# Kernel tuning notes

Measured on AMD Instinct MI355X. Metric: run time of the kernel, lower is better.

## Reference

```python
import jax, jax.numpy as jnp
import numpy as np

N_NODES = 100000
N_EDGES = 640000
HIDDEN = 128
OUT = 128


def _graph_conv(x, edge_index, W_rel, b_rel, W_root):
    # PyG GraphConv (aggr='add'):
    #   out[i] = x[i] @ W_root.T + (sum_{(j->i) in E} x[j]) @ W_rel.T + b_rel
    src, dst = edge_index[0], edge_index[1]
    agg = jax.ops.segment_sum(x[src], dst, num_segments=N_NODES)  # [N, d_in]
    return x @ W_root.T + agg @ W_rel.T + b_rel


def setup_inputs() -> dict:
    key = jax.random.key(0)
    ks = jax.random.split(key, 10)
    x = jax.random.normal(ks[0], (N_NODES, HIDDEN), dtype=jnp.float32)
    edge_index = jax.random.randint(ks[1], (2, N_EDGES), 0, N_NODES, dtype=jnp.int64)
    s = 1.0 / np.sqrt(HIDDEN)
    def w(k, o, i):
        return jax.random.normal(k, (o, i), dtype=jnp.float32) * s
    return {
        "x": x,
        "edge_index": edge_index,
        "W_rel0": w(ks[2], HIDDEN, HIDDEN), "b0": jnp.zeros((HIDDEN,), jnp.float32), "W_root0": w(ks[3], HIDDEN, HIDDEN),
        "W_rel1": w(ks[4], HIDDEN, HIDDEN), "b1": jnp.zeros((HIDDEN,), jnp.float32), "W_root1": w(ks[5], HIDDEN, HIDDEN),
        "W_rel2": w(ks[6], OUT, HIDDEN),    "b2": jnp.zeros((OUT,), jnp.float32),    "W_root2": w(ks[7], OUT, HIDDEN),
    }


def reference(x, edge_index, W_rel0, b0, W_root0, W_rel1, b1, W_root1, W_rel2, b2, W_root2):
    h = jax.nn.relu(_graph_conv(x, edge_index, W_rel0, b0, W_root0))
    h = jax.nn.relu(_graph_conv(h, edge_index, W_rel1, b1, W_root1))
    h = _graph_conv(h, edge_index, W_rel2, b2, W_root2)  # no ReLU on end_conv
    return h
```

## Files before the change

### kernel.cpp

```cpp
#include <hip/hip_runtime.h>

constexpr int HID = 128;

typedef __attribute__((ext_vector_type(8))) short bf16x8;
typedef __attribute__((ext_vector_type(4))) float f32x4;

__device__ __forceinline__ unsigned short f2bf(float f) {
    unsigned int u = __float_as_uint(f);
    u += 0x7fffu + ((u >> 16) & 1u);
    return (unsigned short)(u >> 16);
}
__device__ __forceinline__ float bf_lo(unsigned int v) { return __uint_as_float(v << 16); }
__device__ __forceinline__ float bf_hi(unsigned int v) { return __uint_as_float(v & 0xffff0000u); }

__device__ __forceinline__ void gload16(const void* g, void* l) {
    __builtin_amdgcn_global_load_lds(
        (const __attribute__((address_space(1))) void*)g,
        (__attribute__((address_space(3))) void*)l, 16, 0, 0);
}

__global__ __launch_bounds__(256) void cvt_x_k(
    const float* __restrict__ in, unsigned short* __restrict__ out, int n4)
{
    const int i = blockIdx.x * 256 + threadIdx.x;
    if (i >= n4) return;
    const float4 v = reinterpret_cast<const float4*>(in)[i];
    ushort4 o;
    o.x = f2bf(v.x); o.y = f2bf(v.y); o.z = f2bf(v.z); o.w = f2bf(v.w);
    reinterpret_cast<ushort4*>(out)[i] = o;
}

struct WPtrs { const float* s[6]; unsigned short* d[6]; };
__global__ __launch_bounds__(256) void cvt_w_k(WPtrs p)
{
    const int which = blockIdx.y;
    const int i = blockIdx.x * 256 + threadIdx.x;
    if (i >= (HID * HID) / 4) return;
    const float4 v = reinterpret_cast<const float4*>(p.s[which])[i];
    ushort4 o;
    o.x = f2bf(v.x); o.y = f2bf(v.y); o.z = f2bf(v.z); o.w = f2bf(v.w);
    reinterpret_cast<ushort4*>(p.d[which])[i] = o;
}

__global__ __launch_bounds__(256) void hist_rank_k(
    const int* __restrict__ dst, int* __restrict__ deg,
    int* __restrict__ rank, int nEdges)
{
    const int i = blockIdx.x * blockDim.x + threadIdx.x;
    if (i < nEdges) rank[i] = atomicAdd(&deg[dst[i]], 1);
}

__global__ __launch_bounds__(256) void scan1_k(
    const int* __restrict__ deg, int* __restrict__ part,
    int* __restrict__ blockSums, int n)
{
    __shared__ int s[256];
    const int t = threadIdx.x;
    const int i = blockIdx.x * 1024 + t * 4;
    const int e0 = (i + 0 < n) ? deg[i + 0] : 0;
    const int e1 = (i + 1 < n) ? deg[i + 1] : 0;
    const int e2 = (i + 2 < n) ? deg[i + 2] : 0;
    const int e3 = (i + 3 < n) ? deg[i + 3] : 0;
    const int local = e0 + e1 + e2 + e3;
    s[t] = local;
    __syncthreads();
    for (int off = 1; off < 256; off <<= 1) {
        int v = 0;
        if (t >= off) v = s[t - off];
        __syncthreads();
        if (t >= off) s[t] += v;
        __syncthreads();
    }
    const int incl = s[t];
    int excl = incl - local;
    if (t == 255) blockSums[blockIdx.x] = incl;
    if (i + 0 < n) part[i + 0] = excl; excl += e0;
    if (i + 1 < n) part[i + 1] = excl; excl += e1;
    if (i + 2 < n) part[i + 2] = excl; excl += e2;
    if (i + 3 < n) part[i + 3] = excl;
}

__global__ __launch_bounds__(128) void scan2_k(int* __restrict__ blockSums, int nb)
{
    __shared__ int s[128];
    const int t = threadIdx.x;
    const int v = (t < nb) ? blockSums[t] : 0;
    s[t] = v;
    __syncthreads();
    for (int off = 1; off < 128; off <<= 1) {
        int u = 0;
        if (t >= off) u = s[t - off];
        __syncthreads();
        if (t >= off) s[t] += u;
        __syncthreads();
    }
    if (t < nb) blockSums[t] = s[t] - v;
}

__global__ __launch_bounds__(256) void scan3_k(
    const int* __restrict__ part, const int* __restrict__ blockSums,
    int* __restrict__ rowStart, int n, int nEdges)
{
    const int i = blockIdx.x * blockDim.x + threadIdx.x;
    if (i < n) rowStart[i] = part[i] + blockSums[i >> 10];
    if (i == n) rowStart[n] = nEdges;
}

__global__ __launch_bounds__(256) void fill2_k(
    const int* __restrict__ src, const int* __restrict__ dst,
    const int* __restrict__ rank, const int* __restrict__ rowStart,
    int* __restrict__ eSrc, int nEdges)
{
    const int i = blockIdx.x * blockDim.x + threadIdx.x;
    if (i < nEdges) eSrc[rowStart[dst[i]] + rank[i]] = src[i];
}

__global__ __launch_bounds__(256) void gather_agg_k(
    const unsigned short* __restrict__ feat,
    const int*            __restrict__ rowStart,
    const int*            __restrict__ eSrc,
    unsigned short*       __restrict__ agg,
    int nNodes)
{
    const int wid  = (blockIdx.x * blockDim.x + threadIdx.x) >> 6;
    const int lane = threadIdx.x & 63;
    const int g    = lane >> 4;
    const int sl   = lane & 15;
    const int node = wid * 4 + g;
    if (node >= nNodes) return;

    const int beg = rowStart[node];
    const int end = rowStart[node + 1];
    const size_t colOff = (size_t)sl * 8;
    const int gbase = g << 4;

    float acc[8];
#pragma unroll
    for (int q = 0; q < 8; ++q) acc[q] = 0.f;

    for (int base = beg; base < end; base += 16) {
        const int cnt = min(16, end - base);
        const int si = eSrc[base + min(sl, cnt - 1)];

        int j = 0;
        for (; j + 8 <= cnt; j += 8) {
            uint4 v[8];
#pragma unroll
            for (int q = 0; q < 8; ++q) {
                const int s = __shfl(si, gbase + j + q, 64);
                v[q] = *reinterpret_cast<const uint4*>(feat + (size_t)s * HID + colOff);
            }
#pragma unroll
            for (int q = 0; q < 8; ++q) {
                acc[0] += bf_lo(v[q].x); acc[1] += bf_hi(v[q].x);
                acc[2] += bf_lo(v[q].y); acc[3] += bf_hi(v[q].y);
                acc[4] += bf_lo(v[q].z); acc[5] += bf_hi(v[q].z);
                acc[6] += bf_lo(v[q].w); acc[7] += bf_hi(v[q].w);
            }
        }
        if (j + 4 <= cnt) {
            uint4 v[4];
#pragma unroll
            for (int q = 0; q < 4; ++q) {
                const int s = __shfl(si, gbase + j + q, 64);
                v[q] = *reinterpret_cast<const uint4*>(feat + (size_t)s * HID + colOff);
            }
#pragma unroll
            for (int q = 0; q < 4; ++q) {
                acc[0] += bf_lo(v[q].x); acc[1] += bf_hi(v[q].x);
                acc[2] += bf_lo(v[q].y); acc[3] += bf_hi(v[q].y);
                acc[4] += bf_lo(v[q].z); acc[5] += bf_hi(v[q].z);
                acc[6] += bf_lo(v[q].w); acc[7] += bf_hi(v[q].w);
            }
            j += 4;
        }
        if (j + 2 <= cnt) {
            uint4 v[2];
#pragma unroll
            for (int q = 0; q < 2; ++q) {
                const int s = __shfl(si, gbase + j + q, 64);
                v[q] = *reinterpret_cast<const uint4*>(feat + (size_t)s * HID + colOff);
            }
#pragma unroll
            for (int q = 0; q < 2; ++q) {
                acc[0] += bf_lo(v[q].x); acc[1] += bf_hi(v[q].x);
                acc[2] += bf_lo(v[q].y); acc[3] += bf_hi(v[q].y);
                acc[4] += bf_lo(v[q].z); acc[5] += bf_hi(v[q].z);
                acc[6] += bf_lo(v[q].w); acc[7] += bf_hi(v[q].w);
            }
            j += 2;
        }
        if (j < cnt) {
            const int s = __shfl(si, gbase + j, 64);
            const uint4 v = *reinterpret_cast<const uint4*>(feat + (size_t)s * HID + colOff);
            acc[0] += bf_lo(v.x); acc[1] += bf_hi(v.x);
            acc[2] += bf_lo(v.y); acc[3] += bf_hi(v.y);
            acc[4] += bf_lo(v.z); acc[5] += bf_hi(v.z);
            acc[6] += bf_lo(v.w); acc[7] += bf_hi(v.w);
        }
    }

    uint4 o;
    o.x = (unsigned int)f2bf(acc[0]) | ((unsigned int)f2bf(acc[1]) << 16);
    o.y = (unsigned int)f2bf(acc[2]) | ((unsigned int)f2bf(acc[3]) << 16);
    o.z = (unsigned int)f2bf(acc[4]) | ((unsigned int)f2bf(acc[5]) << 16);
    o.w = (unsigned int)f2bf(acc[6]) | ((unsigned int)f2bf(acc[7]) << 16);
    *reinterpret_cast<uint4*>(agg + (size_t)node * HID + colOff) = o;
}

__device__ __forceinline__ void stage_tile(
    const unsigned short* __restrict__ F, const unsigned short* __restrict__ Wm,
    unsigned short* XsBuf, unsigned short* WsBuf,
    int w, int stHalf, int rsub, int srcColB, int k0, int row0, int rowMax)
{
    if (w < 2) {
#pragma unroll
        for (int q = 0; q < 8; ++q) {
            const int row = stHalf * 64 + q * 8 + rsub;
            const int gr  = min(row0 + row, rowMax);
            gload16((const char*)(F + (size_t)gr * HID + k0) + srcColB,
                    XsBuf + (stHalf * 64 + q * 8) * 64);
        }
    } else {
#pragma unroll
        for (int q = 0; q < 8; ++q) {
            const int row = stHalf * 64 + q * 8 + rsub;
            gload16((const char*)(Wm + (size_t)row * HID + k0) + srcColB,
                    WsBuf + (stHalf * 64 + q * 8) * 64);
        }
    }
}

template <int MODE>
__global__ __launch_bounds__(256) void gemm_mfma_k(
    const unsigned short* __restrict__ X,
    const unsigned short* __restrict__ AGG,
    const unsigned short* __restrict__ Wroot,
    const unsigned short* __restrict__ Wrel,
    const float*          __restrict__ bias,
    void*                 __restrict__ OUTv,
    int nRows)
{
    __shared__ unsigned short Xs[2][128 * 64];
    __shared__ unsigned short Ws[2][128 * 64];

    const int tid  = threadIdx.x;
    const int lane = tid & 63;
    const int w    = tid >> 6;
    const int row0 = blockIdx.x * 128;

    const int wr = w >> 1, wc = w & 1;
    const int R0 = wr * 64, C0 = wc * 64;
    const int lr = lane & 15, lk = lane >> 4;
    const int swz = (lr & 7) << 4;

    const int rsub    = lane >> 3;
    const int srcColB = (((lane & 7) ^ rsub) << 4);
    const int stHalf  = w & 1;
    const int rowMax  = nRows - 1;

    f32x4 acc[4][4];
#pragma unroll
    for (int m = 0; m < 4; ++m)
#pragma unroll
        for (int n = 0; n < 4; ++n) acc[m][n] = f32x4{0.f, 0.f, 0.f, 0.f};

    stage_tile(X, Wroot, Xs[0], Ws[0], w, stHalf, rsub, srcColB, 0, row0, rowMax);

#pragma unroll
    for (int t = 0; t < 4; ++t) {
        const int cur = t & 1;
        if (t < 3) {
            const unsigned short* Fn = (t + 1 < 2) ? X : AGG;
            const unsigned short* Wn = (t + 1 < 2) ? Wroot : Wrel;
            stage_tile(Fn, Wn, Xs[cur ^ 1], Ws[cur ^ 1],
                       w, stHalf, rsub, srcColB, ((t + 1) & 1) * 64, row0, rowMax);
            asm volatile("s_waitcnt vmcnt(8)" ::: "memory");
        } else {
            asm volatile("s_waitcnt vmcnt(0)" ::: "memory");
        }
        __builtin_amdgcn_s_barrier();

#pragma unroll
        for (int ks = 0; ks < 2; ++ks) {
            bf16x8 af[4], bfr[4];
            const int kB = (ks * 64 + lk * 16) ^ swz;
#pragma unroll
            for (int m = 0; m < 4; ++m) {
                const int row = R0 + m * 16 + lr;
                af[m] = *reinterpret_cast<const bf16x8*>((const char*)Xs[cur] + row * 128 + kB);
            }
#pragma unroll
            for (int n = 0; n < 4; ++n) {
                const int col = C0 + n * 16 + lr;
                bfr[n] = *reinterpret_cast<const bf16x8*>((const char*)Ws[cur] + col * 128 + kB);
            }
#pragma unroll
            for (int m = 0; m < 4; ++m)
#pragma unroll
                for (int n = 0; n < 4; ++n)
                    acc[m][n] = __builtin_amdgcn_mfma_f32_16x16x32_bf16(
                        af[m], bfr[n], acc[m][n], 0, 0, 0);
        }
        if (t < 3) __builtin_amdgcn_s_barrier();
    }

    float bv[4];
#pragma unroll
    for (int n = 0; n < 4; ++n) bv[n] = bias[C0 + n * 16 + lr];

#pragma unroll
    for (int m = 0; m < 4; ++m) {
        const int rbase = row0 + R0 + m * 16 + lk * 4;
#pragma unroll
        for (int j = 0; j < 4; ++j) {
            const int r = rbase + j;
            if (r < nRows) {
#pragma unroll
                for (int n = 0; n < 4; ++n) {
                    const int col = C0 + n * 16 + lr;
                    float v = acc[m][n][j] + bv[n];
                    if (MODE == 0) {
                        v = fmaxf(v, 0.f);
                        ((unsigned short*)OUTv)[(size_t)r * HID + col] = f2bf(v);
                    } else {
                        ((float*)OUTv)[(size_t)r * HID + col] = v;
                    }
                }
            }
        }
    }
}

extern "C" void kernel_launch(void* const* d_in, const int* in_sizes, int n_in,
                              void* d_out, int out_size, void* d_ws, size_t ws_size,
                              hipStream_t stream)
{
    const float* x      = (const float*)d_in[0];
    const int*   ei     = (const int*)  d_in[1];
    const float* Wrel0  = (const float*)d_in[2];
    const float* b0     = (const float*)d_in[3];
    const float* Wroot0 = (const float*)d_in[4];
    const float* Wrel1  = (const float*)d_in[5];
    const float* b1     = (const float*)d_in[6];
    const float* Wroot1 = (const float*)d_in[7];
    const float* Wrel2  = (const float*)d_in[8];
    const float* b2     = (const float*)d_in[9];
    const float* Wroot2 = (const float*)d_in[10];

    const int nNodes = in_sizes[0] / HID;
    const int nEdges = in_sizes[1] / 2;
    const int* srcI = ei;
    const int* dstI = ei + nEdges;
    const size_t nF = (size_t)nNodes * HID;

    float* OUT = (float*)d_out;

    unsigned short* xb   = (unsigned short*)d_ws;
    unsigned short* hA   = xb + nF;
    unsigned short* hB   = hA + nF;
    unsigned short* aggb = hB + nF;
    unsigned short* wb   = aggb + nF;
    int* deg       = (int*)(wb + 6 * HID * HID);
    int* part      = deg + nNodes;
    int* rowStart  = part + nNodes;
    int* blockSums = rowStart + nNodes + 1;
    int* rank      = blockSums + 128;
    int* eSrc      = rank + nEdges;

    unsigned short* Wrel0b  = wb + 0 * HID * HID;
    unsigned short* Wroot0b = wb + 1 * HID * HID;
    unsigned short* Wrel1b  = wb + 2 * HID * HID;
    unsigned short* Wroot1b = wb + 3 * HID * HID;
    unsigned short* Wrel2b  = wb + 4 * HID * HID;
    unsigned short* Wroot2b = wb + 5 * HID * HID;

    cvt_x_k<<<(int)((nF / 4 + 255) / 256), 256, 0, stream>>>(x, xb, (int)(nF / 4));
    WPtrs wp;
    wp.s[0] = Wrel0;  wp.d[0] = Wrel0b;
    wp.s[1] = Wroot0; wp.d[1] = Wroot0b;
    wp.s[2] = Wrel1;  wp.d[2] = Wrel1b;
    wp.s[3] = Wroot1; wp.d[3] = Wroot1b;
    wp.s[4] = Wrel2;  wp.d[4] = Wrel2b;
    wp.s[5] = Wroot2; wp.d[5] = Wroot2b;
    cvt_w_k<<<dim3(16, 6), 256, 0, stream>>>(wp);

    const int nb = (nNodes + 1023) / 1024;
    hipMemsetAsync(deg, 0, (size_t)nNodes * sizeof(int), stream);
    hist_rank_k<<<(nEdges + 255) / 256, 256, 0, stream>>>(dstI, deg, rank, nEdges);
    scan1_k<<<nb, 256, 0, stream>>>(deg, part, blockSums, nNodes);
    scan2_k<<<1, 128, 0, stream>>>(blockSums, nb);
    scan3_k<<<(nNodes + 256) / 256, 256, 0, stream>>>(part, blockSums, rowStart, nNodes, nEdges);
    fill2_k<<<(nEdges + 255) / 256, 256, 0, stream>>>(srcI, dstI, rank, rowStart, eSrc, nEdges);

    const int aGrid = (int)(((size_t)(nNodes + 3) / 4 * 64 + 255) / 256);
    const int gGrid = (nNodes + 127) / 128;

    gather_agg_k<<<aGrid, 256, 0, stream>>>(xb, rowStart, eSrc, aggb, nNodes);
    gemm_mfma_k<0><<<gGrid, 256, 0, stream>>>(xb, aggb, Wroot0b, Wrel0b, b0, hA, nNodes);

    gather_agg_k<<<aGrid, 256, 0, stream>>>(hA, rowStart, eSrc, aggb, nNodes);
    gemm_mfma_k<0><<<gGrid, 256, 0, stream>>>(hA, aggb, Wroot1b, Wrel1b, b1, hB, nNodes);

    gather_agg_k<<<aGrid, 256, 0, stream>>>(hB, rowStart, eSrc, aggb, nNodes);
    gemm_mfma_k<1><<<gGrid, 256, 0, stream>>>(hB, aggb, Wroot2b, Wrel2b, b2, OUT, nNodes);
}
```

Before: 206.8 us.

## Fuse neighbor gather into MFMA GEMM and merge prep kernels

```diff
diff --git a/kernel.cpp b/kernel.cpp
--- a/kernel.cpp
+++ b/kernel.cpp
@@ -19,35 +19,36 @@
         (__attribute__((address_space(3))) void*)l, 16, 0, 0);
 }
 
-__global__ __launch_bounds__(256) void cvt_x_k(
-    const float* __restrict__ in, unsigned short* __restrict__ out, int n4)
-{
-    const int i = blockIdx.x * 256 + threadIdx.x;
-    if (i >= n4) return;
-    const float4 v = reinterpret_cast<const float4*>(in)[i];
-    ushort4 o;
-    o.x = f2bf(v.x); o.y = f2bf(v.y); o.z = f2bf(v.z); o.w = f2bf(v.w);
-    reinterpret_cast<ushort4*>(out)[i] = o;
-}
-
-struct WPtrs { const float* s[6]; unsigned short* d[6]; };
-__global__ __launch_bounds__(256) void cvt_w_k(WPtrs p)
-{
-    const int which = blockIdx.y;
-    const int i = blockIdx.x * 256 + threadIdx.x;
-    if (i >= (HID * HID) / 4) return;
-    const float4 v = reinterpret_cast<const float4*>(p.s[which])[i];
-    ushort4 o;
-    o.x = f2bf(v.x); o.y = f2bf(v.y); o.z = f2bf(v.z); o.w = f2bf(v.w);
-    reinterpret_cast<ushort4*>(p.d[which])[i] = o;
-}
-
-__global__ __launch_bounds__(256) void hist_rank_k(
-    const int* __restrict__ dst, int* __restrict__ deg,
-    int* __restrict__ rank, int nEdges)
-{
-    const int i = blockIdx.x * blockDim.x + threadIdx.x;
-    if (i < nEdges) rank[i] = atomicAdd(&deg[dst[i]], 1);
+struct PrepArgs {
+    const int* dst; int* deg; int* rank; int nEdges;
+    const float* ws[6]; unsigned short* wd[6];
+    const float* x; unsigned short* xb; int n4;
+    int histBlocks, cvtwBlocks;
+};
+
+__global__ __launch_bounds__(256) void prep_k(PrepArgs a)
+{
+    const int b   = blockIdx.x;
+    const int tid = threadIdx.x;
+    if (b < a.histBlocks) {
+        const int i = b * 256 + tid;
+        if (i < a.nEdges) a.rank[i] = atomicAdd(&a.deg[a.dst[i]], 1);
+    } else if (b < a.histBlocks + a.cvtwBlocks) {
+        const int idx   = b - a.histBlocks;
+        const int which = idx >> 4;
+        const int i     = (idx & 15) * 256 + tid;
+        const float4 v = reinterpret_cast<const float4*>(a.ws[which])[i];
+        ushort4 o;
+        o.x = f2bf(v.x); o.y = f2bf(v.y); o.z = f2bf(v.z); o.w = f2bf(v.w);
+        reinterpret_cast<ushort4*>(a.wd[which])[i] = o;
+    } else {
+        const int i = (b - a.histBlocks - a.cvtwBlocks) * 256 + tid;
+        if (i >= a.n4) return;
+        const float4 v = reinterpret_cast<const float4*>(a.x)[i];
+        ushort4 o;
+        o.x = f2bf(v.x); o.y = f2bf(v.y); o.z = f2bf(v.z); o.w = f2bf(v.w);
+        reinterpret_cast<ushort4*>(a.xb)[i] = o;
+    }
 }
 
 __global__ __launch_bounds__(256) void scan1_k(
@@ -115,134 +116,20 @@
     if (i < nEdges) eSrc[rowStart[dst[i]] + rank[i]] = src[i];
 }
 
-__global__ __launch_bounds__(256) void gather_agg_k(
-    const unsigned short* __restrict__ feat,
-    const int*            __restrict__ rowStart,
-    const int*            __restrict__ eSrc,
-    unsigned short*       __restrict__ agg,
-    int nNodes)
-{
-    const int wid  = (blockIdx.x * blockDim.x + threadIdx.x) >> 6;
-    const int lane = threadIdx.x & 63;
-    const int g    = lane >> 4;
-    const int sl   = lane & 15;
-    const int node = wid * 4 + g;
-    if (node >= nNodes) return;
-
-    const int beg = rowStart[node];
-    const int end = rowStart[node + 1];
-    const size_t colOff = (size_t)sl * 8;
-    const int gbase = g << 4;
-
-    float acc[8];
-#pragma unroll
-    for (int q = 0; q < 8; ++q) acc[q] = 0.f;
-
-    for (int base = beg; base < end; base += 16) {
-        const int cnt = min(16, end - base);
-        const int si = eSrc[base + min(sl, cnt - 1)];
-
-        int j = 0;
-        for (; j + 8 <= cnt; j += 8) {
-            uint4 v[8];
-#pragma unroll
-            for (int q = 0; q < 8; ++q) {
-                const int s = __shfl(si, gbase + j + q, 64);
-                v[q] = *reinterpret_cast<const uint4*>(feat + (size_t)s * HID + colOff);
-            }
-#pragma unroll
-            for (int q = 0; q < 8; ++q) {
-                acc[0] += bf_lo(v[q].x); acc[1] += bf_hi(v[q].x);
-                acc[2] += bf_lo(v[q].y); acc[3] += bf_hi(v[q].y);
-                acc[4] += bf_lo(v[q].z); acc[5] += bf_hi(v[q].z);
-                acc[6] += bf_lo(v[q].w); acc[7] += bf_hi(v[q].w);
-            }
-        }
-        if (j + 4 <= cnt) {
-            uint4 v[4];
-#pragma unroll
-            for (int q = 0; q < 4; ++q) {
-                const int s = __shfl(si, gbase + j + q, 64);
-                v[q] = *reinterpret_cast<const uint4*>(feat + (size_t)s * HID + colOff);
-            }
-#pragma unroll
-            for (int q = 0; q < 4; ++q) {
-                acc[0] += bf_lo(v[q].x); acc[1] += bf_hi(v[q].x);
-                acc[2] += bf_lo(v[q].y); acc[3] += bf_hi(v[q].y);
-                acc[4] += bf_lo(v[q].z); acc[5] += bf_hi(v[q].z);
-                acc[6] += bf_lo(v[q].w); acc[7] += bf_hi(v[q].w);
-            }
-            j += 4;
-        }
-        if (j + 2 <= cnt) {
-            uint4 v[2];
-#pragma unroll
-            for (int q = 0; q < 2; ++q) {
-                const int s = __shfl(si, gbase + j + q, 64);
-                v[q] = *reinterpret_cast<const uint4*>(feat + (size_t)s * HID + colOff);
-            }
-#pragma unroll
-            for (int q = 0; q < 2; ++q) {
-                acc[0] += bf_lo(v[q].x); acc[1] += bf_hi(v[q].x);
-                acc[2] += bf_lo(v[q].y); acc[3] += bf_hi(v[q].y);
-                acc[4] += bf_lo(v[q].z); acc[5] += bf_hi(v[q].z);
-                acc[6] += bf_lo(v[q].w); acc[7] += bf_hi(v[q].w);
-            }
-            j += 2;
-        }
-        if (j < cnt) {
-            const int s = __shfl(si, gbase + j, 64);
-            const uint4 v = *reinterpret_cast<const uint4*>(feat + (size_t)s * HID + colOff);
-            acc[0] += bf_lo(v.x); acc[1] += bf_hi(v.x);
-            acc[2] += bf_lo(v.y); acc[3] += bf_hi(v.y);
-            acc[4] += bf_lo(v.z); acc[5] += bf_hi(v.z);
-            acc[6] += bf_lo(v.w); acc[7] += bf_hi(v.w);
-        }
-    }
-
-    uint4 o;
-    o.x = (unsigned int)f2bf(acc[0]) | ((unsigned int)f2bf(acc[1]) << 16);
-    o.y = (unsigned int)f2bf(acc[2]) | ((unsigned int)f2bf(acc[3]) << 16);
-    o.z = (unsigned int)f2bf(acc[4]) | ((unsigned int)f2bf(acc[5]) << 16);
-    o.w = (unsigned int)f2bf(acc[6]) | ((unsigned int)f2bf(acc[7]) << 16);
-    *reinterpret_cast<uint4*>(agg + (size_t)node * HID + colOff) = o;
-}
-
-__device__ __forceinline__ void stage_tile(
-    const unsigned short* __restrict__ F, const unsigned short* __restrict__ Wm,
-    unsigned short* XsBuf, unsigned short* WsBuf,
-    int w, int stHalf, int rsub, int srcColB, int k0, int row0, int rowMax)
-{
-    if (w < 2) {
-#pragma unroll
-        for (int q = 0; q < 8; ++q) {
-            const int row = stHalf * 64 + q * 8 + rsub;
-            const int gr  = min(row0 + row, rowMax);
-            gload16((const char*)(F + (size_t)gr * HID + k0) + srcColB,
-                    XsBuf + (stHalf * 64 + q * 8) * 64);
-        }
-    } else {
-#pragma unroll
-        for (int q = 0; q < 8; ++q) {
-            const int row = stHalf * 64 + q * 8 + rsub;
-            gload16((const char*)(Wm + (size_t)row * HID + k0) + srcColB,
-                    WsBuf + (stHalf * 64 + q * 8) * 64);
-        }
-    }
-}
-
 template <int MODE>
-__global__ __launch_bounds__(256) void gemm_mfma_k(
+__global__ __launch_bounds__(256) void gconv_fused_k(
     const unsigned short* __restrict__ X,
-    const unsigned short* __restrict__ AGG,
     const unsigned short* __restrict__ Wroot,
     const unsigned short* __restrict__ Wrel,
     const float*          __restrict__ bias,
+    const int*            __restrict__ rowStart,
+    const int*            __restrict__ eSrc,
     void*                 __restrict__ OUTv,
     int nRows)
 {
-    __shared__ unsigned short Xs[2][128 * 64];
-    __shared__ unsigned short Ws[2][128 * 64];
+    __shared__ unsigned short Xs[128 * 64];
+    __shared__ unsigned short Ws[128 * 64];
+    __shared__ unsigned short As[128 * 128];
 
     const int tid  = threadIdx.x;
     const int lane = tid & 63;
@@ -259,28 +146,120 @@
     const int stHalf  = w & 1;
     const int rowMax  = nRows - 1;
 
+    if (w < 2) {
+#pragma unroll
+        for (int q = 0; q < 8; ++q) {
+            const int row = stHalf * 64 + q * 8 + rsub;
+            const int gr  = min(row0 + row, rowMax);
+            gload16((const char*)(X + (size_t)gr * HID) + srcColB,
+                    Xs + (stHalf * 64 + q * 8) * 64);
+        }
+    } else {
+#pragma unroll
+        for (int q = 0; q < 8; ++q) {
+            const int row = stHalf * 64 + q * 8 + rsub;
+            gload16((const char*)(Wroot + (size_t)row * HID) + srcColB,
+                    Ws + (stHalf * 64 + q * 8) * 64);
+        }
+    }
+
+    {
+        const int g  = lane >> 4;
+        const int sl = lane & 15;
+        const size_t colOff = (size_t)sl * 8;
+        const int gbase = g << 4;
+
+        for (int pass = 0; pass < 8; ++pass) {
+            const int nloc = w * 32 + pass * 4 + g;
+            const int node = row0 + nloc;
+            float acc[8];
+#pragma unroll
+            for (int q = 0; q < 8; ++q) acc[q] = 0.f;
+
+            if (node < nRows) {
+                const int beg = rowStart[node];
+                const int end = rowStart[node + 1];
+                for (int base = beg; base < end; base += 16) {
+                    const int cnt = min(16, end - base);
+                    const int si = eSrc[base + min(sl, cnt - 1)];
+                    int j = 0;
+                    for (; j + 8 <= cnt; j += 8) {
+                        uint4 v[8];
+#pragma unroll
+                        for (int q = 0; q < 8; ++q) {
+                            const int s = __shfl(si, gbase + j + q, 64);
+                            v[q] = *reinterpret_cast<const uint4*>(X + (size_t)s * HID + colOff);
+                        }
+#pragma unroll
+                        for (int q = 0; q < 8; ++q) {
+                            acc[0] += bf_lo(v[q].x); acc[1] += bf_hi(v[q].x);
+                            acc[2] += bf_lo(v[q].y); acc[3] += bf_hi(v[q].y);
+                            acc[4] += bf_lo(v[q].z); acc[5] += bf_hi(v[q].z);
+                            acc[6] += bf_lo(v[q].w); acc[7] += bf_hi(v[q].w);
+                        }
+                    }
+                    if (j + 4 <= cnt) {
+                        uint4 v[4];
+#pragma unroll
+                        for (int q = 0; q < 4; ++q) {
+                            const int s = __shfl(si, gbase + j + q, 64);
+                            v[q] = *reinterpret_cast<const uint4*>(X + (size_t)s * HID + colOff);
+                        }
+#pragma unroll
+                        for (int q = 0; q < 4; ++q) {
+                            acc[0] += bf_lo(v[q].x); acc[1] += bf_hi(v[q].x);
+                            acc[2] += bf_lo(v[q].y); acc[3] += bf_hi(v[q].y);
+                            acc[4] += bf_lo(v[q].z); acc[5] += bf_hi(v[q].z);
+                            acc[6] += bf_lo(v[q].w); acc[7] += bf_hi(v[q].w);
+                        }
+                        j += 4;
+                    }
+                    if (j + 2 <= cnt) {
+                        uint4 v[2];
+#pragma unroll
+                        for (int q = 0; q < 2; ++q) {
+                            const int s = __shfl(si, gbase + j + q, 64);
+                            v[q] = *reinterpret_cast<const uint4*>(X + (size_t)s * HID + colOff);
+                        }
+#pragma unroll
+                        for (int q = 0; q < 2; ++q) {
+                            acc[0] += bf_lo(v[q].x); acc[1] += bf_hi(v[q].x);
+                            acc[2] += bf_lo(v[q].y); acc[3] += bf_hi(v[q].y);
+                            acc[4] += bf_lo(v[q].z); acc[5] += bf_hi(v[q].z);
+                            acc[6] += bf_lo(v[q].w); acc[7] += bf_hi(v[q].w);
+                        }
+                        j += 2;
+                    }
+                    if (j < cnt) {
+                        const int s = __shfl(si, gbase + j, 64);
+                        const uint4 v = *reinterpret_cast<const uint4*>(X + (size_t)s * HID + colOff);
+                        acc[0] += bf_lo(v.x); acc[1] += bf_hi(v.x);
+                        acc[2] += bf_lo(v.y); acc[3] += bf_hi(v.y);
+                        acc[4] += bf_lo(v.z); acc[5] += bf_hi(v.z);
+                        acc[6] += bf_lo(v.w); acc[7] += bf_hi(v.w);
+                    }
+                }
+            }
+            uint4 o;
+            o.x = (unsigned int)f2bf(acc[0]) | ((unsigned int)f2bf(acc[1]) << 16);
+            o.y = (unsigned int)f2bf(acc[2]) | ((unsigned int)f2bf(acc[3]) << 16);
+            o.z = (unsigned int)f2bf(acc[4]) | ((unsigned int)f2bf(acc[5]) << 16);
+            o.w = (unsigned int)f2bf(acc[6]) | ((unsigned int)f2bf(acc[7]) << 16);
+            const int colB = (sl * 16) ^ ((nloc & 7) << 4);
+            *reinterpret_cast<uint4*>((char*)As + nloc * 256 + colB) = o;
+        }
+    }
+
+    __syncthreads();
+
     f32x4 acc[4][4];
 #pragma unroll
     for (int m = 0; m < 4; ++m)
 #pragma unroll
         for (int n = 0; n < 4; ++n) acc[m][n] = f32x4{0.f, 0.f, 0.f, 0.f};
 
-    stage_tile(X, Wroot, Xs[0], Ws[0], w, stHalf, rsub, srcColB, 0, row0, rowMax);
-
 #pragma unroll
     for (int t = 0; t < 4; ++t) {
-        const int cur = t & 1;
-        if (t < 3) {
-            const unsigned short* Fn = (t + 1 < 2) ? X : AGG;
-            const unsigned short* Wn = (t + 1 < 2) ? Wroot : Wrel;
-            stage_tile(Fn, Wn, Xs[cur ^ 1], Ws[cur ^ 1],
-                       w, stHalf, rsub, srcColB, ((t + 1) & 1) * 64, row0, rowMax);
-            asm volatile("s_waitcnt vmcnt(8)" ::: "memory");
-        } else {
-            asm volatile("s_waitcnt vmcnt(0)" ::: "memory");
-        }
-        __builtin_amdgcn_s_barrier();
-
 #pragma unroll
         for (int ks = 0; ks < 2; ++ks) {
             bf16x8 af[4], bfr[4];
@@ -288,12 +267,17 @@
 #pragma unroll
             for (int m = 0; m < 4; ++m) {
                 const int row = R0 + m * 16 + lr;
-                af[m] = *reinterpret_cast<const bf16x8*>((const char*)Xs[cur] + row * 128 + kB);
+                if (t < 2) {
+                    af[m] = *reinterpret_cast<const bf16x8*>((const char*)Xs + row * 128 + kB);
+                } else {
+                    const int cB = ((t - 2) * 128 + ks * 64 + lk * 16) ^ ((row & 7) << 4);
+                    af[m] = *reinterpret_cast<const bf16x8*>((const char*)As + row * 256 + cB);
+                }
             }
 #pragma unroll
             for (int n = 0; n < 4; ++n) {
                 const int col = C0 + n * 16 + lr;
-                bfr[n] = *reinterpret_cast<const bf16x8*>((const char*)Ws[cur] + col * 128 + kB);
+                bfr[n] = *reinterpret_cast<const bf16x8*>((const char*)Ws + col * 128 + kB);
             }
 #pragma unroll
             for (int m = 0; m < 4; ++m)
@@ -302,7 +286,39 @@
                     acc[m][n] = __builtin_amdgcn_mfma_f32_16x16x32_bf16(
                         af[m], bfr[n], acc[m][n], 0, 0, 0);
         }
-        if (t < 3) __builtin_amdgcn_s_barrier();
+
+        if (t < 3) {
+            __syncthreads();
+            if (t == 0) {
+                if (w < 2) {
+#pragma unroll
+                    for (int q = 0; q < 8; ++q) {
+                        const int row = stHalf * 64 + q * 8 + rsub;
+                        const int gr  = min(row0 + row, rowMax);
+                        gload16((const char*)(X + (size_t)gr * HID + 64) + srcColB,
+                                Xs + (stHalf * 64 + q * 8) * 64);
+                    }
+                } else {
+#pragma unroll
+                    for (int q = 0; q < 8; ++q) {
+                        const int row = stHalf * 64 + q * 8 + rsub;
+                        gload16((const char*)(Wroot + (size_t)row * HID + 64) + srcColB,
+                                Ws + (stHalf * 64 + q * 8) * 64);
+                    }
+                }
+            } else {
+                const int k0 = (t - 1) * 64;
+                if (w >= 2) {
+#pragma unroll
+                    for (int q = 0; q < 8; ++q) {
+                        const int row = stHalf * 64 + q * 8 + rsub;
+                        gload16((const char*)(Wrel + (size_t)row * HID + k0) + srcColB,
+                                Ws + (stHalf * 64 + q * 8) * 64);
+                    }
+                }
+            }
+            __syncthreads();
+        }
     }
 
     float bv[4];
@@ -359,8 +375,7 @@
     unsigned short* xb   = (unsigned short*)d_ws;
     unsigned short* hA   = xb + nF;
     unsigned short* hB   = hA + nF;
-    unsigned short* aggb = hB + nF;
-    unsigned short* wb   = aggb + nF;
+    unsigned short* wb   = hB + nF;
     int* deg       = (int*)(wb + 6 * HID * HID);
     int* part      = deg + nNodes;
     int* rowStart  = part + nNodes;
@@ -375,33 +390,30 @@
     unsigned short* Wrel2b  = wb + 4 * HID * HID;
     unsigned short* Wroot2b = wb + 5 * HID * HID;
 
-    cvt_x_k<<<(int)((nF / 4 + 255) / 256), 256, 0, stream>>>(x, xb, (int)(nF / 4));
-    WPtrs wp;
-    wp.s[0] = Wrel0;  wp.d[0] = Wrel0b;
-    wp.s[1] = Wroot0; wp.d[1] = Wroot0b;
-    wp.s[2] = Wrel1;  wp.d[2] = Wrel1b;
-    wp.s[3] = Wroot1; wp.d[3] = Wroot1b;
-    wp.s[4] = Wrel2;  wp.d[4] = Wrel2b;
-    wp.s[5] = Wroot2; wp.d[5] = Wroot2b;
-    cvt_w_k<<<dim3(16, 6), 256, 0, stream>>>(wp);
+    hipMemsetAsync(deg, 0, (size_t)nNodes * sizeof(int), stream);
+    PrepArgs pa;
+    pa.dst = dstI; pa.deg = deg; pa.rank = rank; pa.nEdges = nEdges;
+    pa.ws[0] = Wrel0;  pa.wd[0] = Wrel0b;
+    pa.ws[1] = Wroot0; pa.wd[1] = Wroot0b;
+    pa.ws[2] = Wrel1;  pa.wd[2] = Wrel1b;
+    pa.ws[3] = Wroot1; pa.wd[3] = Wroot1b;
+    pa.ws[4] = Wrel2;  pa.wd[4] = Wrel2b;
+    pa.ws[5] = Wroot2; pa.wd[5] = Wroot2b;
+    pa.x = x; pa.xb = xb; pa.n4 = (int)(nF / 4);
+    pa.histBlocks = (nEdges + 255) / 256;
+    pa.cvtwBlocks = 96;
+    const int prepGrid = pa.histBlocks + pa.cvtwBlocks + (pa.n4 + 255) / 256;
+    prep_k<<<prepGrid, 256, 0, stream>>>(pa);
 
     const int nb = (nNodes + 1023) / 1024;
-    hipMemsetAsync(deg, 0, (size_t)nNodes * sizeof(int), stream);
-    hist_rank_k<<<(nEdges + 255) / 256, 256, 0, stream>>>(dstI, deg, rank, nEdges);
     scan1_k<<<nb, 256, 0, stream>>>(deg, part, blockSums, nNodes);
     scan2_k<<<1, 128, 0, stream>>>(blockSums, nb);
     scan3_k<<<(nNodes + 256) / 256, 256, 0, stream>>>(part, blockSums, rowStart, nNodes, nEdges);
     fill2_k<<<(nEdges + 255) / 256, 256, 0, stream>>>(srcI, dstI, rank, rowStart, eSrc, nEdges);
 
-    const int aGrid = (int)(((size_t)(nNodes + 3) / 4 * 64 + 255) / 256);
     const int gGrid = (nNodes + 127) / 128;
 
-    gather_agg_k<<<aGrid, 256, 0, stream>>>(xb, rowStart, eSrc, aggb, nNodes);
-    gemm_mfma_k<0><<<gGrid, 256, 0, stream>>>(xb, aggb, Wroot0b, Wrel0b, b0, hA, nNodes);
-
-    gather_agg_k<<<aGrid, 256, 0, stream>>>(hA, rowStart, eSrc, aggb, nNodes);
-    gemm_mfma_k<0><<<gGrid, 256, 0, stream>>>(hA, aggb, Wroot1b, Wrel1b, b1, hB, nNodes);
-
-    gather_agg_k<<<aGrid, 256, 0, stream>>>(hB, rowStart, eSrc, aggb, nNodes);
-    gemm_mfma_k<1><<<gGrid, 256, 0, stream>>>(hB, aggb, Wroot2b, Wrel2b, b2, OUT, nNodes);
-}
+    gconv_fused_k<0><<<gGrid, 256, 0, stream>>>(xb, Wroot0b, Wrel0b, b0, rowStart, eSrc, hA, nNodes);
+    gconv_fused_k<0><<<gGrid, 256, 0, stream>>>(hA, Wroot1b, Wrel1b, b1, rowStart, eSrc, hB, nNodes);
+    gconv_fused_k<1><<<gGrid, 256, 0, stream>>>(hB, Wroot2b, Wrel2b, b2, rowStart, eSrc, OUT, nNodes);
+}
```

Measured after the change: 239.9 us. +16.0%, slower.
